# Kernel tuning notes

Hardware: AMD Instinct MI355X
Metric: run time of the kernel (lower is better)

## Reference

```python
import jax, jax.numpy as jnp
import numpy as np

NUM_ENT = 50000
NUM_REL = 64
NUM_TRI = 400000
DIN = 128
DOUT = 128
DREL = 128
NUM_HEAD = 8
DH = DOUT // NUM_HEAD


def setup_inputs() -> dict:
    key = jax.random.key(0)
    ks = jax.random.split(key, 9)
    emb_ent = jax.random.normal(ks[0], (NUM_ENT, DIN), jnp.float32)
    emb_rel = jax.random.normal(ks[1], (NUM_REL, DREL), jnp.float32)
    heads = jax.random.randint(ks[2], (NUM_TRI,), 0, NUM_ENT)
    rels = jax.random.randint(ks[3], (NUM_TRI,), 0, NUM_REL)
    tails = jax.random.randint(ks[4], (NUM_TRI,), 0, NUM_ENT)
    triplets = jnp.stack([heads, rels, tails], axis=-1)
    # xavier-normal-like init (stored as [in, out]; torch Linear applies x @ W.T)
    Wa = jax.random.normal(ks[5], (2 * DIN + DREL, DOUT), jnp.float32) * (2.0 / (2 * DIN + DREL + DOUT)) ** 0.5
    ba = jnp.zeros((DOUT,), jnp.float32)
    attn_vec = jax.random.normal(ks[6], (1, NUM_HEAD, DH), jnp.float32) * 0.1
    Wg = jax.random.normal(ks[7], (DIN + DREL, DOUT), jnp.float32) * (2.0 / (DIN + DREL + DOUT)) ** 0.5
    bg = jnp.zeros((DOUT,), jnp.float32)
    return {"emb_ent": emb_ent, "emb_rel": emb_rel, "triplets": triplets,
            "Wa": Wa, "ba": ba, "attn_vec": attn_vec, "Wg": Wg, "bg": bg}


def reference(emb_ent, emb_rel, triplets, Wa, ba, attn_vec, Wg, bg):
    num_ent = emb_ent.shape[0]
    n_head, d_hid = attn_vec.shape[1], attn_vec.shape[2]
    head, rel, tail = triplets[:, 0], triplets[:, 1], triplets[:, 2]

    # in-degree of each entity (as attention-softmax denominator for self_rel)
    ent_freq = jax.ops.segment_sum(jnp.ones(tail.shape, jnp.float32), tail,
                                   num_segments=num_ent)[:, None]
    # torch adds 1e-16 to all entries iff any entry is zero
    ent_freq = ent_freq + jnp.where(jnp.any(ent_freq == 0.0), 1e-16, 0.0)

    # mean relation embedding of incoming edges per entity -> self-loop relation
    self_rel = jax.ops.segment_sum(emb_rel[rel], tail, num_segments=num_ent) / ent_freq

    # append self-loops: one per entity
    emb_rels = jnp.concatenate([emb_rel[rel], self_rel], axis=0)       # [E+N, dr]
    ar = jnp.arange(num_ent)
    head_all = jnp.concatenate([head, ar], axis=0)                     # [E+N]
    tail_all = jnp.concatenate([tail, ar], axis=0)                     # [E+N]

    # attention logits per edge per head
    feat_att = jnp.concatenate([emb_ent[tail_all], emb_ent[head_all], emb_rels], axis=-1)
    h = jnp.tanh(feat_att @ Wa + ba).reshape(-1, n_head, d_hid)
    attn_raw = jnp.sum(h * attn_vec, axis=-1, keepdims=True)           # [E+N, H, 1]

    # segment softmax over edges sharing a tail (every segment has a self-loop)
    amax = jax.ops.segment_max(attn_raw, tail_all, num_segments=num_ent)
    attn_val = jnp.exp(attn_raw - amax[tail_all])
    asum = jax.ops.segment_sum(attn_val, tail_all, num_segments=num_ent)
    beta = attn_val / (asum[tail_all] + 1e-16)                         # [E+N, H, 1]

    # message projection and weighted aggregation
    msg = (jnp.concatenate([emb_ent[head_all], emb_rels], axis=-1) @ Wg + bg)
    msg = msg.reshape(-1, n_head, d_hid)
    out = jax.ops.segment_sum(beta * msg, tail_all, num_segments=num_ent)
    return out.reshape(num_ent, -1)
```

## Files before the change

kernel.cpp:

```cpp
#include <hip/hip_runtime.h>
#include <math.h>

#define NUM_ENT  50000
#define NUM_REL  64
#define NUM_TRI  400000
#define DIN      128
#define CAP      64

#define DEGS     16

#define PACK_BLOCKS  24
#define SMALL_BLOCKS 64
#define PREP_BLOCKS  (PACK_BLOCKS + SMALL_BLOCKS)

#define ENT_BLOCKS   782
#define SCAT_BLOCKS  391
#define MID_BLOCKS   (ENT_BLOCKS + SCAT_BLOCKS)

typedef __attribute__((ext_vector_type(8))) short bf16x8;
typedef __attribute__((ext_vector_type(8))) unsigned short u16x8;
typedef __attribute__((ext_vector_type(4))) float f32x4;

__device__ __forceinline__ float4 f4add(float4 a, float4 b) {
    return make_float4(a.x + b.x, a.y + b.y, a.z + b.z, a.w + b.w);
}

__device__ __forceinline__ unsigned short f2bf(float f) {
    unsigned u = __float_as_uint(f);
    unsigned r = ((u >> 16) & 1u) + 0x7fffu;
    return (unsigned short)((u + r) >> 16);
}
__device__ __forceinline__ float bf2f(unsigned short h) {
    return __uint_as_float(((unsigned)h) << 16);
}
__device__ __forceinline__ float4 ldbf4(const unsigned short* p) {
    ushort4 u = *(const ushort4*)p;
    return make_float4(bf2f(u.x), bf2f(u.y), bf2f(u.z), bf2f(u.w));
}
__device__ __forceinline__ void ldbf8(const unsigned short* p, float4* lo, float4* hi) {
    u16x8 u = *(const u16x8*)p;
    *lo = make_float4(bf2f(u[0]), bf2f(u[1]), bf2f(u[2]), bf2f(u[3]));
    *hi = make_float4(bf2f(u[4]), bf2f(u[5]), bf2f(u[6]), bf2f(u[7]));
}

__device__ __forceinline__ float att_p(float4 x, float4 m2av, float sumAv) {
    float r0 = __builtin_amdgcn_rcpf(__expf(2.f * x.x) + 1.f);
    float r1 = __builtin_amdgcn_rcpf(__expf(2.f * x.y) + 1.f);
    float r2 = __builtin_amdgcn_rcpf(__expf(2.f * x.z) + 1.f);
    float r3 = __builtin_amdgcn_rcpf(__expf(2.f * x.w) + 1.f);
    return fmaf(m2av.x, r0, fmaf(m2av.y, r1, fmaf(m2av.z, r2, fmaf(m2av.w, r3, sumAv))));
}

__global__ __launch_bounds__(256) void k_prep(const float* __restrict__ emb_rel,
                                              const float* __restrict__ Wa,
                                              const float* __restrict__ Wg,
                                              unsigned short* __restrict__ Bpack,
                                              unsigned short* __restrict__ TaTg) {
    __shared__ float s[DIN];
    int b = blockIdx.x;
    int tid = threadIdx.x;

    if (b < PACK_BLOCKS) {
        for (int i = 0; i < 8; i++) {
            int idx = b * 2048 + i * 256 + tid;
            int j    = idx & 7;
            int lane = (idx >> 3) & 63;
            int ks   = (idx >> 9) & 3;
            int t    = (idx >> 11) & 7;
            int w    = idx >> 14;
            int k = ks * 32 + ((lane >> 4) << 3) + j;
            int n = t * 16 + (lane & 15);
            const float* W = (w == 0) ? Wa : (w == 1) ? (Wa + 128 * DIN) : Wg;
            Bpack[idx] = f2bf(W[k * DIN + n]);
        }
    } else {
        int row = b - PACK_BLOCKS;
        if (tid < DIN) s[tid] = emb_rel[row * DIN + tid];
        __syncthreads();
        int j = tid & 127;
        const float* W = (tid < 128) ? (Wa + 256 * DIN) : (Wg + 128 * DIN);
        float acc = 0.f;
#pragma unroll 8
        for (int k = 0; k < DIN; k++) acc += s[k] * W[k * DIN + j];
        int pos = row * 256 + 8 * (j >> 2) + (j & 3) + ((tid < 128) ? 0 : 4);
        TaTg[pos] = f2bf(acc);
    }
}

__global__ __launch_bounds__(256) void k_mid(const float* __restrict__ X,
                                             const unsigned short* __restrict__ Bpack,
                                             const int* __restrict__ trip,
                                             const float* __restrict__ ba,
                                             const float* __restrict__ bg,
                                             unsigned short* __restrict__ Pt,
                                             unsigned short* __restrict__ PhGh,
                                             int* __restrict__ deg,
                                             int* __restrict__ elist) {
    __shared__ unsigned short As[64][136];
    int b = blockIdx.x;
    int tid = threadIdx.x;

    if (b < ENT_BLOCKS) {
        int m0 = b * 64;
        for (int i = 0; i < 8; i++) {
            int v = tid + i * 256;
            int row = v >> 5;
            int c4 = v & 31;
            int gr = m0 + row;
            if (gr >= NUM_ENT) gr = NUM_ENT - 1;
            float4 x = *(const float4*)&X[gr * DIN + c4 * 4];
            ushort4 h;
            h.x = f2bf(x.x); h.y = f2bf(x.y); h.z = f2bf(x.z); h.w = f2bf(x.w);
            *(ushort4*)&As[row][c4 * 4] = h;
        }
        __syncthreads();

        int w = tid >> 6;
        int q = tid & 63;
        int quad = q >> 4;
        int lrow = w * 16 + (q & 15);
        int gr = m0 + lrow;

        bf16x8 a[4];
#pragma unroll
        for (int ks = 0; ks < 4; ks++)
            a[ks] = *(const bf16x8*)&As[lrow][ks * 32 + quad * 8];

        const bf16x8* Bp = (const bf16x8*)Bpack;
#pragma unroll
        for (int s = 0; s < 3; s++) {
            f32x4 acc[8];
#pragma unroll
            for (int t = 0; t < 8; t++) acc[t] = (f32x4){0.f, 0.f, 0.f, 0.f};
#pragma unroll
            for (int ks = 0; ks < 4; ks++) {
#pragma unroll
                for (int t = 0; t < 8; t++) {
                    bf16x8 wf = Bp[((s * 8 + t) * 4 + ks) * 64 + q];
                    acc[t] = __builtin_amdgcn_mfma_f32_16x16x32_bf16(wf, a[ks], acc[t], 0, 0, 0);
                }
            }
            if (gr < NUM_ENT) {
#pragma unroll
                for (int t = 0; t < 8; t++) {
                    int n0 = t * 16 + quad * 4;
                    float4 bb = make_float4(0.f, 0.f, 0.f, 0.f);
                    if (s == 0) bb = *(const float4*)&ba[n0];
                    if (s == 2) bb = *(const float4*)&bg[n0];
                    ushort4 o;
                    o.x = f2bf(acc[t][0] + bb.x);
                    o.y = f2bf(acc[t][1] + bb.y);
                    o.z = f2bf(acc[t][2] + bb.z);
                    o.w = f2bf(acc[t][3] + bb.w);
                    if (s == 0) {
                        *(ushort4*)&Pt[gr * DIN + n0] = o;
                    } else {
                        *(ushort4*)&PhGh[gr * 256 + 2 * n0 + ((s == 1) ? 0 : 4)] = o;
                    }
                }
            }
        }
    } else {
        int i0 = (b - ENT_BLOCKS) * 1024 + tid * 4;
        if (i0 < NUM_TRI) {
            const int4* tp = (const int4*)&trip[i0 * 3];
            int4 A = tp[0], B4 = tp[1], C4 = tp[2];
            int hs[4] = {A.x, A.w, B4.z, C4.y};
            int rs[4] = {A.y, B4.x, B4.w, C4.z};
            int ts[4] = {A.z, B4.y, C4.x, C4.w};
#pragma unroll
            for (int u = 0; u < 4; u++) {
                int pos = atomicAdd(&deg[ts[u] * DEGS], 1);
                if (pos < CAP) elist[ts[u] * CAP + pos] = (hs[u] << 6) | rs[u];
            }
        }
    }
}

__global__ __launch_bounds__(256) void k_fused(const int* __restrict__ elist,
                                               const int* __restrict__ deg_arr,
                                               const unsigned short* __restrict__ Pt,
                                               const unsigned short* __restrict__ PhGh,
                                               const unsigned short* __restrict__ TaTg,
                                               const float* __restrict__ attn_vec,
                                               float* __restrict__ out) {
    int tid = threadIdx.x;
    int wv = tid >> 6;
    int lane = tid & 63;
    int half = lane >> 5;
    int q = lane & 31;
    int t = blockIdx.x * 4 + wv;
    int deg = deg_arr[t * DEGS];
    if (deg > CAP) deg = CAP;
    int c = q * 4;

    float4 pt4 = ldbf4(&Pt[t * DIN + c]);
    float4 av4 = *(const float4*)&attn_vec[c];
    float sumAv = av4.x + av4.y + av4.z + av4.w;
    float4 m2av = make_float4(-2.f * av4.x, -2.f * av4.y, -2.f * av4.z, -2.f * av4.w);

    int eall = elist[t * CAP + lane];

    float l = 0.f;
    float4 acc = make_float4(0.f, 0.f, 0.f, 0.f);
    float4 sTa = make_float4(0.f, 0.f, 0.f, 0.f);
    float4 sTg = make_float4(0.f, 0.f, 0.f, 0.f);

    int it = half;
    for (; it + 2 < deg; it += 4) {
        int e0 = __shfl(eall, it);
        int e1 = __shfl(eall, it + 2);
        int h0 = e0 >> 6, r0 = e0 & 63;
        int h1 = e1 >> 6, r1 = e1 & 63;
        float4 ta0, tg0, ph0, gh0, ta1, tg1, ph1, gh1;
        ldbf8(&TaTg[r0 * 256 + q * 8], &ta0, &tg0);
        ldbf8(&PhGh[h0 * 256 + q * 8], &ph0, &gh0);
        ldbf8(&TaTg[r1 * 256 + q * 8], &ta1, &tg1);
        ldbf8(&PhGh[h1 * 256 + q * 8], &ph1, &gh1);

        sTa = f4add(sTa, f4add(ta0, ta1));
        sTg = f4add(sTg, f4add(tg0, tg1));
        float4 pa0 = f4add(ph0, ta0);
        float4 gm0 = f4add(gh0, tg0);
        float4 pa1 = f4add(ph1, ta1);
        float4 gm1 = f4add(gh1, tg1);
        float p0 = att_p(f4add(pt4, pa0), m2av, sumAv);
        float p1 = att_p(f4add(pt4, pa1), m2av, sumAv);
        p0 += __shfl_xor(p0, 1);
        p0 += __shfl_xor(p0, 2);
        p1 += __shfl_xor(p1, 1);
        p1 += __shfl_xor(p1, 2);
        float w0 = __expf(p0);
        float w1 = __expf(p1);
        l += w0 + w1;
        acc.x += w0 * gm0.x + w1 * gm1.x;
        acc.y += w0 * gm0.y + w1 * gm1.y;
        acc.z += w0 * gm0.z + w1 * gm1.z;
        acc.w += w0 * gm0.w + w1 * gm1.w;
    }
    {
        int e = __shfl(eall, it & (CAP - 1));
        if (it < deg) {
            int h = e >> 6;
            int r = e & 63;
            float4 ta, tg, ph, gh;
            ldbf8(&TaTg[r * 256 + q * 8], &ta, &tg);
            ldbf8(&PhGh[h * 256 + q * 8], &ph, &gh);
            sTa = f4add(sTa, ta);
            sTg = f4add(sTg, tg);
            float4 pa = f4add(ph, ta);
            float4 gm = f4add(gh, tg);
            float p = att_p(f4add(pt4, pa), m2av, sumAv);
            p += __shfl_xor(p, 1);
            p += __shfl_xor(p, 2);
            float w = __expf(p);
            l += w;
            acc.x += w * gm.x; acc.y += w * gm.y; acc.z += w * gm.z; acc.w += w * gm.w;
        }
    }

    l     += __shfl_xor(l, 32);
    acc.x += __shfl_xor(acc.x, 32);
    acc.y += __shfl_xor(acc.y, 32);
    acc.z += __shfl_xor(acc.z, 32);
    acc.w += __shfl_xor(acc.w, 32);
    sTa.x += __shfl_xor(sTa.x, 32);
    sTa.y += __shfl_xor(sTa.y, 32);
    sTa.z += __shfl_xor(sTa.z, 32);
    sTa.w += __shfl_xor(sTa.w, 32);
    sTg.x += __shfl_xor(sTg.x, 32);
    sTg.y += __shfl_xor(sTg.y, 32);
    sTg.z += __shfl_xor(sTg.z, 32);
    sTg.w += __shfl_xor(sTg.w, 32);

    {
        float inv = (deg > 0) ? __builtin_amdgcn_rcpf((float)deg) : 0.f;
        float4 pa, gm;
        ldbf8(&PhGh[t * 256 + q * 8], &pa, &gm);
        pa.x += sTa.x * inv; pa.y += sTa.y * inv; pa.z += sTa.z * inv; pa.w += sTa.w * inv;
        gm.x += sTg.x * inv; gm.y += sTg.y * inv; gm.z += sTg.z * inv; gm.w += sTg.w * inv;
        float p = att_p(f4add(pt4, pa), m2av, sumAv);
        p += __shfl_xor(p, 1);
        p += __shfl_xor(p, 2);
        float w = __expf(p);
        l += w;
        acc.x += w * gm.x; acc.y += w * gm.y; acc.z += w * gm.z; acc.w += w * gm.w;
    }
    float invl = 1.f / (l + 1e-16f);
    if (half == 0) {
        *(float4*)&out[t * DIN + c] =
            make_float4(acc.x * invl, acc.y * invl, acc.z * invl, acc.w * invl);
    }
}

extern "C" void kernel_launch(void* const* d_in, const int* in_sizes, int n_in,
                              void* d_out, int out_size, void* d_ws, size_t ws_size,
                              hipStream_t stream) {
    const float* emb_ent  = (const float*)d_in[0];
    const float* emb_rel  = (const float*)d_in[1];
    const int*   trip     = (const int*)d_in[2];
    const float* Wa       = (const float*)d_in[3];
    const float* ba       = (const float*)d_in[4];
    const float* attn_vec = (const float*)d_in[5];
    const float* Wg       = (const float*)d_in[6];
    const float* bg       = (const float*)d_in[7];
    float* out = (float*)d_out;

    unsigned short* wsh = (unsigned short*)d_ws;
    unsigned short* Pt    = wsh;
    unsigned short* PhGh  = wsh + 6400000;
    unsigned short* TaTg  = wsh + 19200000;
    unsigned short* Bpack = wsh + 19216384;
    int* deg   = (int*)(wsh + 19265536);
    int* elist = deg + 50000 * DEGS;

    hipMemsetAsync(deg, 0, NUM_ENT * DEGS * sizeof(int), stream);

    k_prep<<<PREP_BLOCKS, 256, 0, stream>>>(emb_rel, Wa, Wg, Bpack, TaTg);

    k_mid<<<MID_BLOCKS, 256, 0, stream>>>(emb_ent, Bpack, trip, ba, bg,
                                          Pt, PhGh, deg, elist);

    k_fused<<<NUM_ENT / 4, 256, 0, stream>>>(elist, deg,
                                             Pt, PhGh, TaTg, attn_vec, out);
}
```

Baseline: 184.3 us.

## Pack degree counters densely, zero them in prep kernel, interleave scatter blocks

Removes the 16-int padding on per-entity degree counters so they become a dense array, and drops the separate memset by zeroing the counters in extra blocks of the prep kernel. The mid kernel now interleaves scatter blocks with GEMM tiles (one scatter block per two tiles) so atomics overlap with matrix work instead of running at the end. The dense layout may add atomic contention on shared cache lines, but it cuts memset traffic and one launch.

```diff
diff --git a/kernel.cpp b/kernel.cpp
--- a/kernel.cpp
+++ b/kernel.cpp
@@ -7,15 +7,14 @@
 #define DIN      128
 #define CAP      64
 
-#define DEGS     16
-
 #define PACK_BLOCKS  24
 #define SMALL_BLOCKS 64
-#define PREP_BLOCKS  (PACK_BLOCKS + SMALL_BLOCKS)
-
+#define ZERO_BLOCKS  196
+#define PREP_BLOCKS  (PACK_BLOCKS + SMALL_BLOCKS + ZERO_BLOCKS)
+
+#define SCAT_BLOCKS  391
 #define ENT_BLOCKS   782
-#define SCAT_BLOCKS  391
-#define MID_BLOCKS   (ENT_BLOCKS + SCAT_BLOCKS)
+#define MID_BLOCKS   (SCAT_BLOCKS + ENT_BLOCKS)
 
 typedef __attribute__((ext_vector_type(8))) short bf16x8;
 typedef __attribute__((ext_vector_type(8))) unsigned short u16x8;
@@ -55,7 +54,8 @@
                                               const float* __restrict__ Wa,
                                               const float* __restrict__ Wg,
                                               unsigned short* __restrict__ Bpack,
-                                              unsigned short* __restrict__ TaTg) {
+                                              unsigned short* __restrict__ TaTg,
+                                              int* __restrict__ deg) {
     __shared__ float s[DIN];
     int b = blockIdx.x;
     int tid = threadIdx.x;
@@ -73,7 +73,7 @@
             const float* W = (w == 0) ? Wa : (w == 1) ? (Wa + 128 * DIN) : Wg;
             Bpack[idx] = f2bf(W[k * DIN + n]);
         }
-    } else {
+    } else if (b < PACK_BLOCKS + SMALL_BLOCKS) {
         int row = b - PACK_BLOCKS;
         if (tid < DIN) s[tid] = emb_rel[row * DIN + tid];
         __syncthreads();
@@ -84,6 +84,9 @@
         for (int k = 0; k < DIN; k++) acc += s[k] * W[k * DIN + j];
         int pos = row * 256 + 8 * (j >> 2) + (j & 3) + ((tid < 128) ? 0 : 4);
         TaTg[pos] = f2bf(acc);
+    } else {
+        int idx = (b - PACK_BLOCKS - SMALL_BLOCKS) * 256 + tid;
+        if (idx < NUM_ENT) deg[idx] = 0;
     }
 }
 
@@ -99,9 +102,26 @@
     __shared__ unsigned short As[64][136];
     int b = blockIdx.x;
     int tid = threadIdx.x;
-
-    if (b < ENT_BLOCKS) {
-        int m0 = b * 64;
+    int third = b / 3;
+    int rem = b - third * 3;
+
+    if (rem == 0) {
+        int i0 = third * 1024 + tid * 4;
+        if (i0 < NUM_TRI) {
+            const int4* tp = (const int4*)&trip[i0 * 3];
+            int4 A = tp[0], B4 = tp[1], C4 = tp[2];
+            int hs[4] = {A.x, A.w, B4.z, C4.y};
+            int rs[4] = {A.y, B4.x, B4.w, C4.z};
+            int ts[4] = {A.z, B4.y, C4.x, C4.w};
+#pragma unroll
+            for (int u = 0; u < 4; u++) {
+                int pos = atomicAdd(&deg[ts[u]], 1);
+                if (pos < CAP) elist[ts[u] * CAP + pos] = (hs[u] << 6) | rs[u];
+            }
+        }
+    } else {
+        int tile = third * 2 + rem - 1;
+        int m0 = tile * 64;
         for (int i = 0; i < 8; i++) {
             int v = tid + i * 256;
             int row = v >> 5;
@@ -160,20 +180,6 @@
                 }
             }
         }
-    } else {
-        int i0 = (b - ENT_BLOCKS) * 1024 + tid * 4;
-        if (i0 < NUM_TRI) {
-            const int4* tp = (const int4*)&trip[i0 * 3];
-            int4 A = tp[0], B4 = tp[1], C4 = tp[2];
-            int hs[4] = {A.x, A.w, B4.z, C4.y};
-            int rs[4] = {A.y, B4.x, B4.w, C4.z};
-            int ts[4] = {A.z, B4.y, C4.x, C4.w};
-#pragma unroll
-            for (int u = 0; u < 4; u++) {
-                int pos = atomicAdd(&deg[ts[u] * DEGS], 1);
-                if (pos < CAP) elist[ts[u] * CAP + pos] = (hs[u] << 6) | rs[u];
-            }
-        }
     }
 }
 
@@ -190,7 +196,7 @@
     int half = lane >> 5;
     int q = lane & 31;
     int t = blockIdx.x * 4 + wv;
-    int deg = deg_arr[t * DEGS];
+    int deg = deg_arr[t];
     if (deg > CAP) deg = CAP;
     int c = q * 4;
 
@@ -312,11 +318,9 @@
     unsigned short* TaTg  = wsh + 19200000;
     unsigned short* Bpack = wsh + 19216384;
     int* deg   = (int*)(wsh + 19265536);
-    int* elist = deg + 50000 * DEGS;
-
-    hipMemsetAsync(deg, 0, NUM_ENT * DEGS * sizeof(int), stream);
-
-    k_prep<<<PREP_BLOCKS, 256, 0, stream>>>(emb_rel, Wa, Wg, Bpack, TaTg);
+    int* elist = deg + 50000;
+
+    k_prep<<<PREP_BLOCKS, 256, 0, stream>>>(emb_rel, Wa, Wg, Bpack, TaTg, deg);
 
     k_mid<<<MID_BLOCKS, 256, 0, stream>>>(emb_ent, Bpack, trip, ba, bg,
                                           Pt, PhGh, deg, elist);
```

Result: faster. 172.6 us (-6.3%).
